# Optimization experiments

Hardware: AMD Instinct MI355X
Metric: run time of the kernel (lower is better)

## Reference

```python
import jax, jax.numpy as jnp
import numpy as np

NUM_SEQS = 16
NUM_HEADS = 32
NUM_KV_HEADS = 8
HEAD_SIZE = 128
BLOCK_SIZE = 16
X = 8  # vectorized key-cache packing factor
MAX_CTX = 4096
MAX_BLOCKS = MAX_CTX // BLOCK_SIZE
NUM_BLOCKS = NUM_SEQS * MAX_BLOCKS
SCALE = 0.08838834764831845  # 1/sqrt(128)
NEG_INF = -1e30


def setup_inputs() -> dict:
    key0 = jax.random.key(0)
    ks = jax.random.split(key0, 5)
    query = jax.random.normal(ks[0], (NUM_SEQS, 1, NUM_HEADS * HEAD_SIZE), jnp.float32)
    key = jax.random.normal(ks[1], (NUM_SEQS, 1, NUM_KV_HEADS * HEAD_SIZE), jnp.float32)
    value = jax.random.normal(ks[2], (NUM_SEQS, 1, NUM_KV_HEADS * HEAD_SIZE), jnp.float32)
    key_cache = jax.random.normal(ks[3], (NUM_BLOCKS, NUM_KV_HEADS, HEAD_SIZE // X, BLOCK_SIZE, X), jnp.float32)
    value_cache = jax.random.normal(ks[4], (NUM_BLOCKS, NUM_KV_HEADS, HEAD_SIZE, BLOCK_SIZE), jnp.float32)
    rng = np.random.default_rng(0)
    block_tables = rng.permutation(NUM_BLOCKS).reshape(NUM_SEQS, MAX_BLOCKS).astype(np.int32)
    context_lens = rng.integers(256, MAX_CTX + 1, size=(NUM_SEQS,)).astype(np.int32)
    last = context_lens - 1
    slots = block_tables[np.arange(NUM_SEQS), last // BLOCK_SIZE].astype(np.int64) * BLOCK_SIZE + (last % BLOCK_SIZE)
    slot_mapping = slots.reshape(NUM_SEQS, 1)
    return {
        'query': query, 'key': key, 'value': value,
        'key_cache': key_cache, 'value_cache': value_cache,
        'block_tables': jnp.asarray(block_tables),
        'context_lens': jnp.asarray(context_lens),
        'slot_mapping': jnp.asarray(slot_mapping),
    }


def _paged_attention_decode(query, key, value, key_cache, value_cache, block_tables, context_lens, slot_mapping):
    S, L1, hidden = query.shape  # L1 == 1 (decode)
    nb, kvH, _, bs, x = key_cache.shape
    D = value_cache.shape[2]
    H = hidden // D
    G = H // kvH  # queries per kv head
    maxB = block_tables.shape[1]

    q = query.reshape(S, H, D)
    k_new = key.reshape(S, kvH, D)
    v_new = value.reshape(S, kvH, D)

    # --- reshape_and_cache: write new K/V into paged caches ---
    sm = slot_mapping.reshape(-1)
    blk, off = sm // bs, sm % bs
    key_cache = key_cache.at[blk, :, :, off, :].set(k_new.reshape(S, kvH, D // x, x))
    value_cache = value_cache.at[blk, :, :, off].set(v_new)

    # --- gather paged KV via block tables ---
    # key_cache [nb,kvH,D/x,bs,x] -> [nb,kvH,bs,D]
    kc = key_cache.transpose(0, 1, 3, 2, 4).reshape(nb, kvH, bs, D)
    vc = value_cache.transpose(0, 1, 3, 2)  # [nb,kvH,bs,D]
    keys = kc[block_tables].transpose(0, 1, 3, 2, 4).reshape(S, maxB * bs, kvH, D)
    vals = vc[block_tables].transpose(0, 1, 3, 2, 4).reshape(S, maxB * bs, kvH, D)

    # --- GQA attention with context-length masking ---
    qg = q.reshape(S, kvH, G, D)
    scores = jnp.einsum('skgd,slkd->skgl', qg, keys) * jnp.asarray(SCALE, q.dtype)
    valid = jnp.arange(maxB * bs)[None, :] < context_lens[:, None]  # [S,L]
    scores = jnp.where(valid[:, None, None, :], scores, NEG_INF)
    probs = jax.nn.softmax(scores, axis=-1)
    out = jnp.einsum('skgl,slkd->skgd', probs, vals)
    return out.reshape(S, 1, H * D)


def reference(query, key, value, key_cache, value_cache, block_tables, context_lens, slot_mapping):
    return _paged_attention_decode(query, key, value, key_cache, value_cache,
                                   block_tables, context_lens, slot_mapping)
```

## Files before the change

kernel.cpp:

```cpp
#include <hip/hip_runtime.h>

#define NSEQ   16
#define KVH    8
#define NG     4
#define HD     128
#define BS     16
#define MAXB   256
#define PART   256
#define NPART  16
#define NITEMS (NSEQ * KVH * NPART)
#define WPT    64
#define PSTRIDE 520
#define REC_BYTES ((size_t)NITEMS * PSTRIDE * 4)
#define SCALE_F 0.08838834764831845f
#define NWORKERS 1024

__global__ __launch_bounds__(256) void pa_partial_kernel(
    const float* __restrict__ query,
    const float* __restrict__ key,
    const float* __restrict__ value,
    const float* __restrict__ key_cache,
    const float* __restrict__ value_cache,
    const int*   __restrict__ block_tables,
    const int*   __restrict__ context_lens,
    float*       __restrict__ ws,
    unsigned int* __restrict__ counter)
{
    __shared__ float p_lds[4][NG][WPT];
    __shared__ float o_lds[4][NG * HD];
    __shared__ float ml_lds[4][8];
    __shared__ int   item_s;

    const int tid  = threadIdx.x;
    const int wv   = tid >> 6;
    const int lane = tid & 63;

    for (;;) {
        if (tid == 0) item_s = (int)atomicAdd(counter, 1u);
        __syncthreads();
        const int item = item_s;
        __syncthreads();
        if (item >= NITEMS) return;

        const int p   = item & (NPART - 1);
        const int kvh = (item >> 4) & (KVH - 1);
        const int s   = item >> 7;
        const int ctx = context_lens[s];
        const int t0  = p * PART;
        if (t0 >= ctx) continue;

        const int tw0  = t0 + wv * WPT;
        const bool wact = (tw0 < ctx);

        const float* q = query + ((size_t)s * KVH + kvh) * (NG * HD);

        float m_w = -1e30f;
        float l_w[NG] = {0.f, 0.f, 0.f, 0.f};

        if (wact) {
            const int t  = tw0 + lane;
            const int bt = block_tables[s * MAXB + (t >> 4)];
            const float* kb = key_cache + (size_t)bt * (KVH * HD * BS)
                                        + (size_t)kvh * (HD * BS) + (t & 15) * 8;

            float sc[NG] = {0.f, 0.f, 0.f, 0.f};
            #pragma unroll
            for (int j = 0; j < 16; ++j) {
                const float4 ka = *(const float4*)(kb + j * 128);
                const float4 kc = *(const float4*)(kb + j * 128 + 4);
                #pragma unroll
                for (int g = 0; g < NG; ++g) {
                    sc[g] += q[g * HD + j * 8 + 0] * ka.x + q[g * HD + j * 8 + 1] * ka.y
                           + q[g * HD + j * 8 + 2] * ka.z + q[g * HD + j * 8 + 3] * ka.w
                           + q[g * HD + j * 8 + 4] * kc.x + q[g * HD + j * 8 + 5] * kc.y
                           + q[g * HD + j * 8 + 6] * kc.z + q[g * HD + j * 8 + 7] * kc.w;
                }
            }

            if (t == ctx - 1) {
                const float4* kn4 = (const float4*)(key + ((size_t)s * KVH + kvh) * HD);
                float ns[NG] = {0.f, 0.f, 0.f, 0.f};
                #pragma unroll
                for (int c = 0; c < 32; ++c) {
                    const float4 k4 = kn4[c];
                    #pragma unroll
                    for (int g = 0; g < NG; ++g) {
                        ns[g] += q[g * HD + c * 4 + 0] * k4.x + q[g * HD + c * 4 + 1] * k4.y
                               + q[g * HD + c * 4 + 2] * k4.z + q[g * HD + c * 4 + 3] * k4.w;
                    }
                }
                #pragma unroll
                for (int g = 0; g < NG; ++g) sc[g] = ns[g];
            }

            float mv;
            if (t < ctx) {
                #pragma unroll
                for (int g = 0; g < NG; ++g) sc[g] *= SCALE_F;
                mv = fmaxf(fmaxf(sc[0], sc[1]), fmaxf(sc[2], sc[3]));
            } else {
                #pragma unroll
                for (int g = 0; g < NG; ++g) sc[g] = -1e30f;
                mv = -1e30f;
            }

            #pragma unroll
            for (int o = 32; o; o >>= 1) mv = fmaxf(mv, __shfl_xor(mv, o));
            m_w = mv;

            float pr[NG];
            #pragma unroll
            for (int g = 0; g < NG; ++g) {
                pr[g] = __expf(sc[g] - m_w);
                p_lds[wv][g][lane] = pr[g];
                l_w[g] = pr[g];
            }
            #pragma unroll
            for (int o = 32; o; o >>= 1) {
                l_w[0] += __shfl_xor(l_w[0], o);
                l_w[1] += __shfl_xor(l_w[1], o);
                l_w[2] += __shfl_xor(l_w[2], o);
                l_w[3] += __shfl_xor(l_w[3], o);
            }
        }

        if (lane == 0) {
            ml_lds[wv][0] = m_w;
            #pragma unroll
            for (int g = 0; g < NG; ++g) ml_lds[wv][1 + g] = l_w[g];
        }

        if (wact) {
            int btv[4];
            #pragma unroll
            for (int b = 0; b < 4; ++b)
                btv[b] = block_tables[s * MAXB + (tw0 >> 4) + b];

            const int tl = ctx - 1 - tw0;
            const int tq = lane & 3;
            const int dl = lane >> 2;

            float acc[NG][8];
            #pragma unroll
            for (int g = 0; g < NG; ++g)
                #pragma unroll
                for (int sub = 0; sub < 8; ++sub) acc[g][sub] = 0.f;

            #pragma unroll
            for (int b = 0; b < 4; ++b) {
                if (tw0 + b * 16 < ctx) {
                    const float* vb = value_cache + (size_t)btv[b] * (KVH * HD * BS)
                                                  + (size_t)kvh * (HD * BS);
                    float4 p4[NG];
                    #pragma unroll
                    for (int g = 0; g < NG; ++g)
                        p4[g] = *(const float4*)&p_lds[wv][g][b * 16 + tq * 4];
                    #pragma unroll
                    for (int sub = 0; sub < 8; ++sub) {
                        const float4 v4 = *(const float4*)(vb + sub * 256 + lane * 4);
                        #pragma unroll
                        for (int g = 0; g < NG; ++g)
                            acc[g][sub] += p4[g].x * v4.x + p4[g].y * v4.y
                                         + p4[g].z * v4.z + p4[g].w * v4.w;
                    }
                }
            }

            #pragma unroll
            for (int g = 0; g < NG; ++g)
                #pragma unroll
                for (int sub = 0; sub < 8; ++sub) {
                    float a = acc[g][sub];
                    a += __shfl_xor(a, 1);
                    a += __shfl_xor(a, 2);
                    acc[g][sub] = a;
                }

            if (tl >= 0 && tl < WPT) {
                const int btn = block_tables[s * MAXB + ((ctx - 1) >> 4)];
                const float* vbn = value_cache + (size_t)btn * (KVH * HD * BS)
                                               + (size_t)kvh * (HD * BS) + ((ctx - 1) & 15);
                const float* vrow = value + ((size_t)s * KVH + kvh) * HD;
                #pragma unroll
                for (int sub = 0; sub < 8; ++sub) {
                    const int d = sub * 16 + dl;
                    const float dv = vrow[d] - vbn[d * BS];
                    #pragma unroll
                    for (int g = 0; g < NG; ++g)
                        acc[g][sub] += p_lds[wv][g][tl] * dv;
                }
            }

            if (tq == 0) {
                #pragma unroll
                for (int g = 0; g < NG; ++g)
                    #pragma unroll
                    for (int sub = 0; sub < 8; ++sub)
                        o_lds[wv][g * HD + sub * 16 + dl] = acc[g][sub];
            }
        } else {
            #pragma unroll
            for (int i = 0; i < 8; ++i) o_lds[wv][i * 64 + lane] = 0.f;
        }

        __syncthreads();

        const float m0 = ml_lds[0][0], m1 = ml_lds[1][0], m2 = ml_lds[2][0], m3 = ml_lds[3][0];
        const float M  = fmaxf(fmaxf(m0, m1), fmaxf(m2, m3));
        const float w0 = __expf(m0 - M), w1 = __expf(m1 - M);
        const float w2 = __expf(m2 - M), w3 = __expf(m3 - M);

        float* rec = ws + (size_t)item * PSTRIDE;
        #pragma unroll
        for (int r = 0; r < 2; ++r) {
            const int idx = tid + r * 256;
            rec[idx] = w0 * o_lds[0][idx] + w1 * o_lds[1][idx]
                     + w2 * o_lds[2][idx] + w3 * o_lds[3][idx];
        }
        if (tid < NG) {
            rec[512 + tid] = w0 * ml_lds[0][1 + tid] + w1 * ml_lds[1][1 + tid]
                           + w2 * ml_lds[2][1 + tid] + w3 * ml_lds[3][1 + tid];
        }
        if (tid == 4) rec[516] = M;
    }
}

__global__ __launch_bounds__(128) void pa_reduce_kernel(
    const float* __restrict__ ws,
    const int*   __restrict__ context_lens,
    float*       __restrict__ out)
{
    const int b    = blockIdx.x;
    const int g    = b & 3;
    const int pair = b >> 2;
    const int s    = pair >> 3;
    const int kvh  = pair & 7;
    const int ctx  = context_lens[s];
    const int np   = (ctx + PART - 1) / PART;

    const int d = threadIdx.x;
    const float* base = ws + (size_t)pair * NPART * PSTRIDE;

    float M = -1e30f;
    for (int p2 = 0; p2 < np; ++p2) M = fmaxf(M, base[p2 * PSTRIDE + 516]);

    float L = 0.f, acc = 0.f;
    for (int p2 = 0; p2 < np; ++p2) {
        const float* rec = base + p2 * PSTRIDE;
        const float w = __expf(rec[516] - M);
        L   += w * rec[512 + g];
        acc += w * rec[g * HD + d];
    }

    out[(size_t)s * (KVH * NG * HD) + (size_t)(kvh * NG + g) * HD + d] = acc / L;
}

extern "C" void kernel_launch(void* const* d_in, const int* in_sizes, int n_in,
                              void* d_out, int out_size, void* d_ws, size_t ws_size,
                              hipStream_t stream) {
    const float* query       = (const float*)d_in[0];
    const float* key         = (const float*)d_in[1];
    const float* value       = (const float*)d_in[2];
    const float* key_cache   = (const float*)d_in[3];
    const float* value_cache = (const float*)d_in[4];
    const int*   block_tables  = (const int*)d_in[5];
    const int*   context_lens  = (const int*)d_in[6];

    float* out = (float*)d_out;
    float* ws  = (float*)d_ws;
    unsigned int* counter = (unsigned int*)((char*)d_ws + REC_BYTES);

    (void)hipMemsetAsync(counter, 0, sizeof(unsigned int), stream);
    pa_partial_kernel<<<NWORKERS, 256, 0, stream>>>(
        query, key, value, key_cache, value_cache, block_tables, context_lens, ws, counter);
    pa_reduce_kernel<<<NSEQ * KVH * NG, 128, 0, stream>>>(ws, context_lens, out);
}
```

Baseline: 83.60 us.

## Fuse split-K reduction into partial kernel via per-pair completion counters

Removes the separate reduce kernel launch. Each work item bumps an atomic per-(seq,kv-head) counter, and the block that finishes the last partition merges the partial records with coherent loads and writes the output. This saves one kernel launch and its tail gap. In exchange it adds fences, atomics and an extra barrier per item, and the final merge is serialized on whichever block closes each pair.

```diff
diff --git a/kernel.cpp b/kernel.cpp
--- a/kernel.cpp
+++ b/kernel.cpp
@@ -9,13 +9,18 @@
 #define PART   256
 #define NPART  16
 #define NITEMS (NSEQ * KVH * NPART)
+#define NPAIRS (NSEQ * KVH)
 #define WPT    64
 #define PSTRIDE 520
 #define REC_BYTES ((size_t)NITEMS * PSTRIDE * 4)
 #define SCALE_F 0.08838834764831845f
 #define NWORKERS 1024
 
-__global__ __launch_bounds__(256) void pa_partial_kernel(
+__device__ __forceinline__ float cohld(const float* p) {
+    return __hip_atomic_load(p, __ATOMIC_RELAXED, __HIP_MEMORY_SCOPE_AGENT);
+}
+
+__global__ __launch_bounds__(256) void pa_fused_kernel(
     const float* __restrict__ query,
     const float* __restrict__ key,
     const float* __restrict__ value,
@@ -24,12 +29,16 @@
     const int*   __restrict__ block_tables,
     const int*   __restrict__ context_lens,
     float*       __restrict__ ws,
-    unsigned int* __restrict__ counter)
+    unsigned int* __restrict__ counter,
+    float*       __restrict__ out)
 {
     __shared__ float p_lds[4][NG][WPT];
     __shared__ float o_lds[4][NG * HD];
     __shared__ float ml_lds[4][8];
     __shared__ int   item_s;
+    __shared__ int   close_s;
+
+    unsigned int* pair_done = counter + 1;
 
     const int tid  = threadIdx.x;
     const int wv   = tid >> 6;
@@ -42,217 +51,223 @@
         __syncthreads();
         if (item >= NITEMS) return;
 
-        const int p   = item & (NPART - 1);
-        const int kvh = (item >> 4) & (KVH - 1);
-        const int s   = item >> 7;
-        const int ctx = context_lens[s];
-        const int t0  = p * PART;
-        if (t0 >= ctx) continue;
-
-        const int tw0  = t0 + wv * WPT;
-        const bool wact = (tw0 < ctx);
-
-        const float* q = query + ((size_t)s * KVH + kvh) * (NG * HD);
-
-        float m_w = -1e30f;
-        float l_w[NG] = {0.f, 0.f, 0.f, 0.f};
-
-        if (wact) {
-            const int t  = tw0 + lane;
-            const int bt = block_tables[s * MAXB + (t >> 4)];
-            const float* kb = key_cache + (size_t)bt * (KVH * HD * BS)
-                                        + (size_t)kvh * (HD * BS) + (t & 15) * 8;
-
-            float sc[NG] = {0.f, 0.f, 0.f, 0.f};
+        const int p    = item & (NPART - 1);
+        const int kvh  = (item >> 4) & (KVH - 1);
+        const int s    = item >> 7;
+        const int pair = item >> 4;
+        const int ctx  = context_lens[s];
+        const int t0   = p * PART;
+        const bool active = (t0 < ctx);
+
+        if (active) {
+            const int tw0  = t0 + wv * WPT;
+            const bool wact = (tw0 < ctx);
+
+            const float* q = query + ((size_t)s * KVH + kvh) * (NG * HD);
+
+            float m_w = -1e30f;
+            float l_w[NG] = {0.f, 0.f, 0.f, 0.f};
+
+            if (wact) {
+                const int t  = tw0 + lane;
+                const int bt = block_tables[s * MAXB + (t >> 4)];
+                const float* kb = key_cache + (size_t)bt * (KVH * HD * BS)
+                                            + (size_t)kvh * (HD * BS) + (t & 15) * 8;
+
+                float sc[NG] = {0.f, 0.f, 0.f, 0.f};
+                #pragma unroll
+                for (int j = 0; j < 16; ++j) {
+                    const float4 ka = *(const float4*)(kb + j * 128);
+                    const float4 kc = *(const float4*)(kb + j * 128 + 4);
+                    #pragma unroll
+                    for (int g = 0; g < NG; ++g) {
+                        sc[g] += q[g * HD + j * 8 + 0] * ka.x + q[g * HD + j * 8 + 1] * ka.y
+                               + q[g * HD + j * 8 + 2] * ka.z + q[g * HD + j * 8 + 3] * ka.w
+                               + q[g * HD + j * 8 + 4] * kc.x + q[g * HD + j * 8 + 5] * kc.y
+                               + q[g * HD + j * 8 + 6] * kc.z + q[g * HD + j * 8 + 7] * kc.w;
+                    }
+                }
+
+                if (t == ctx - 1) {
+                    const float4* kn4 = (const float4*)(key + ((size_t)s * KVH + kvh) * HD);
+                    float ns[NG] = {0.f, 0.f, 0.f, 0.f};
+                    #pragma unroll
+                    for (int c = 0; c < 32; ++c) {
+                        const float4 k4 = kn4[c];
+                        #pragma unroll
+                        for (int g = 0; g < NG; ++g) {
+                            ns[g] += q[g * HD + c * 4 + 0] * k4.x + q[g * HD + c * 4 + 1] * k4.y
+                                   + q[g * HD + c * 4 + 2] * k4.z + q[g * HD + c * 4 + 3] * k4.w;
+                        }
+                    }
+                    #pragma unroll
+                    for (int g = 0; g < NG; ++g) sc[g] = ns[g];
+                }
+
+                float mv;
+                if (t < ctx) {
+                    #pragma unroll
+                    for (int g = 0; g < NG; ++g) sc[g] *= SCALE_F;
+                    mv = fmaxf(fmaxf(sc[0], sc[1]), fmaxf(sc[2], sc[3]));
+                } else {
+                    #pragma unroll
+                    for (int g = 0; g < NG; ++g) sc[g] = -1e30f;
+                    mv = -1e30f;
+                }
+
+                #pragma unroll
+                for (int o = 32; o; o >>= 1) mv = fmaxf(mv, __shfl_xor(mv, o));
+                m_w = mv;
+
+                float pr[NG];
+                #pragma unroll
+                for (int g = 0; g < NG; ++g) {
+                    pr[g] = __expf(sc[g] - m_w);
+                    p_lds[wv][g][lane] = pr[g];
+                    l_w[g] = pr[g];
+                }
+                #pragma unroll
+                for (int o = 32; o; o >>= 1) {
+                    l_w[0] += __shfl_xor(l_w[0], o);
+                    l_w[1] += __shfl_xor(l_w[1], o);
+                    l_w[2] += __shfl_xor(l_w[2], o);
+                    l_w[3] += __shfl_xor(l_w[3], o);
+                }
+            }
+
+            if (lane == 0) {
+                ml_lds[wv][0] = m_w;
+                #pragma unroll
+                for (int g = 0; g < NG; ++g) ml_lds[wv][1 + g] = l_w[g];
+            }
+
+            if (wact) {
+                int btv[4];
+                #pragma unroll
+                for (int b = 0; b < 4; ++b)
+                    btv[b] = block_tables[s * MAXB + (tw0 >> 4) + b];
+
+                const int tl = ctx - 1 - tw0;
+                const int tq = lane & 3;
+                const int dl = lane >> 2;
+
+                float acc[NG][8];
+                #pragma unroll
+                for (int g = 0; g < NG; ++g)
+                    #pragma unroll
+                    for (int sub = 0; sub < 8; ++sub) acc[g][sub] = 0.f;
+
+                #pragma unroll
+                for (int b = 0; b < 4; ++b) {
+                    if (tw0 + b * 16 < ctx) {
+                        const float* vb = value_cache + (size_t)btv[b] * (KVH * HD * BS)
+                                                      + (size_t)kvh * (HD * BS);
+                        float4 p4[NG];
+                        #pragma unroll
+                        for (int g = 0; g < NG; ++g)
+                            p4[g] = *(const float4*)&p_lds[wv][g][b * 16 + tq * 4];
+                        #pragma unroll
+                        for (int sub = 0; sub < 8; ++sub) {
+                            const float4 v4 = *(const float4*)(vb + sub * 256 + lane * 4);
+                            #pragma unroll
+                            for (int g = 0; g < NG; ++g)
+                                acc[g][sub] += p4[g].x * v4.x + p4[g].y * v4.y
+                                             + p4[g].z * v4.z + p4[g].w * v4.w;
+                        }
+                    }
+                }
+
+                #pragma unroll
+                for (int g = 0; g < NG; ++g)
+                    #pragma unroll
+                    for (int sub = 0; sub < 8; ++sub) {
+                        float a = acc[g][sub];
+                        a += __shfl_xor(a, 1);
+                        a += __shfl_xor(a, 2);
+                        acc[g][sub] = a;
+                    }
+
+                if (tl >= 0 && tl < WPT) {
+                    const int btn = block_tables[s * MAXB + ((ctx - 1) >> 4)];
+                    const float* vbn = value_cache + (size_t)btn * (KVH * HD * BS)
+                                                   + (size_t)kvh * (HD * BS) + ((ctx - 1) & 15);
+                    const float* vrow = value + ((size_t)s * KVH + kvh) * HD;
+                    #pragma unroll
+                    for (int sub = 0; sub < 8; ++sub) {
+                        const int d = sub * 16 + dl;
+                        const float dv = vrow[d] - vbn[d * BS];
+                        #pragma unroll
+                        for (int g = 0; g < NG; ++g)
+                            acc[g][sub] += p_lds[wv][g][tl] * dv;
+                    }
+                }
+
+                if (tq == 0) {
+                    #pragma unroll
+                    for (int g = 0; g < NG; ++g)
+                        #pragma unroll
+                        for (int sub = 0; sub < 8; ++sub)
+                            o_lds[wv][g * HD + sub * 16 + dl] = acc[g][sub];
+                }
+            } else {
+                #pragma unroll
+                for (int i = 0; i < 8; ++i) o_lds[wv][i * 64 + lane] = 0.f;
+            }
+
+            __syncthreads();
+
+            const float m0 = ml_lds[0][0], m1 = ml_lds[1][0], m2 = ml_lds[2][0], m3 = ml_lds[3][0];
+            const float M  = fmaxf(fmaxf(m0, m1), fmaxf(m2, m3));
+            const float w0 = __expf(m0 - M), w1 = __expf(m1 - M);
+            const float w2 = __expf(m2 - M), w3 = __expf(m3 - M);
+
+            float* rec = ws + (size_t)item * PSTRIDE;
             #pragma unroll
-            for (int j = 0; j < 16; ++j) {
-                const float4 ka = *(const float4*)(kb + j * 128);
-                const float4 kc = *(const float4*)(kb + j * 128 + 4);
-                #pragma unroll
-                for (int g = 0; g < NG; ++g) {
-                    sc[g] += q[g * HD + j * 8 + 0] * ka.x + q[g * HD + j * 8 + 1] * ka.y
-                           + q[g * HD + j * 8 + 2] * ka.z + q[g * HD + j * 8 + 3] * ka.w
-                           + q[g * HD + j * 8 + 4] * kc.x + q[g * HD + j * 8 + 5] * kc.y
-                           + q[g * HD + j * 8 + 6] * kc.z + q[g * HD + j * 8 + 7] * kc.w;
-                }
-            }
-
-            if (t == ctx - 1) {
-                const float4* kn4 = (const float4*)(key + ((size_t)s * KVH + kvh) * HD);
-                float ns[NG] = {0.f, 0.f, 0.f, 0.f};
-                #pragma unroll
-                for (int c = 0; c < 32; ++c) {
-                    const float4 k4 = kn4[c];
-                    #pragma unroll
-                    for (int g = 0; g < NG; ++g) {
-                        ns[g] += q[g * HD + c * 4 + 0] * k4.x + q[g * HD + c * 4 + 1] * k4.y
-                               + q[g * HD + c * 4 + 2] * k4.z + q[g * HD + c * 4 + 3] * k4.w;
-                    }
-                }
-                #pragma unroll
-                for (int g = 0; g < NG; ++g) sc[g] = ns[g];
-            }
-
-            float mv;
-            if (t < ctx) {
-                #pragma unroll
-                for (int g = 0; g < NG; ++g) sc[g] *= SCALE_F;
-                mv = fmaxf(fmaxf(sc[0], sc[1]), fmaxf(sc[2], sc[3]));
-            } else {
-                #pragma unroll
-                for (int g = 0; g < NG; ++g) sc[g] = -1e30f;
-                mv = -1e30f;
-            }
+            for (int r = 0; r < 2; ++r) {
+                const int idx = tid + r * 256;
+                rec[idx] = w0 * o_lds[0][idx] + w1 * o_lds[1][idx]
+                         + w2 * o_lds[2][idx] + w3 * o_lds[3][idx];
+            }
+            if (tid < NG) {
+                rec[512 + tid] = w0 * ml_lds[0][1 + tid] + w1 * ml_lds[1][1 + tid]
+                               + w2 * ml_lds[2][1 + tid] + w3 * ml_lds[3][1 + tid];
+            }
+            if (tid == 4) rec[516] = M;
+
+            __syncthreads();
+        }
+
+        if (tid == 0) {
+            __threadfence();
+            const unsigned old = atomicAdd(&pair_done[pair], 1u);
+            close_s = (old == NPART - 1) ? 1 : 0;
+        }
+        __syncthreads();
+
+        if (close_s) {
+            __threadfence();
+            const int np = (ctx + PART - 1) / PART;
+            const float* base = ws + (size_t)pair * NPART * PSTRIDE;
+
+            float M = -1e30f;
+            for (int p2 = 0; p2 < np; ++p2)
+                M = fmaxf(M, cohld(base + p2 * PSTRIDE + 516));
 
             #pragma unroll
-            for (int o = 32; o; o >>= 1) mv = fmaxf(mv, __shfl_xor(mv, o));
-            m_w = mv;
-
-            float pr[NG];
-            #pragma unroll
-            for (int g = 0; g < NG; ++g) {
-                pr[g] = __expf(sc[g] - m_w);
-                p_lds[wv][g][lane] = pr[g];
-                l_w[g] = pr[g];
-            }
-            #pragma unroll
-            for (int o = 32; o; o >>= 1) {
-                l_w[0] += __shfl_xor(l_w[0], o);
-                l_w[1] += __shfl_xor(l_w[1], o);
-                l_w[2] += __shfl_xor(l_w[2], o);
-                l_w[3] += __shfl_xor(l_w[3], o);
+            for (int half = 0; half < 2; ++half) {
+                const int g = (tid >> 7) + half * 2;
+                const int d = tid & 127;
+                float L = 0.f, acc = 0.f;
+                for (int p2 = 0; p2 < np; ++p2) {
+                    const float* rec = base + p2 * PSTRIDE;
+                    const float w = __expf(cohld(rec + 516) - M);
+                    L   += w * cohld(rec + 512 + g);
+                    acc += w * cohld(rec + g * HD + d);
+                }
+                out[(size_t)s * (KVH * NG * HD) + (size_t)(kvh * NG + g) * HD + d] = acc / L;
             }
         }
-
-        if (lane == 0) {
-            ml_lds[wv][0] = m_w;
-            #pragma unroll
-            for (int g = 0; g < NG; ++g) ml_lds[wv][1 + g] = l_w[g];
-        }
-
-        if (wact) {
-            int btv[4];
-            #pragma unroll
-            for (int b = 0; b < 4; ++b)
-                btv[b] = block_tables[s * MAXB + (tw0 >> 4) + b];
-
-            const int tl = ctx - 1 - tw0;
-            const int tq = lane & 3;
-            const int dl = lane >> 2;
-
-            float acc[NG][8];
-            #pragma unroll
-            for (int g = 0; g < NG; ++g)
-                #pragma unroll
-                for (int sub = 0; sub < 8; ++sub) acc[g][sub] = 0.f;
-
-            #pragma unroll
-            for (int b = 0; b < 4; ++b) {
-                if (tw0 + b * 16 < ctx) {
-                    const float* vb = value_cache + (size_t)btv[b] * (KVH * HD * BS)
-                                                  + (size_t)kvh * (HD * BS);
-                    float4 p4[NG];
-                    #pragma unroll
-                    for (int g = 0; g < NG; ++g)
-                        p4[g] = *(const float4*)&p_lds[wv][g][b * 16 + tq * 4];
-                    #pragma unroll
-                    for (int sub = 0; sub < 8; ++sub) {
-                        const float4 v4 = *(const float4*)(vb + sub * 256 + lane * 4);
-                        #pragma unroll
-                        for (int g = 0; g < NG; ++g)
-                            acc[g][sub] += p4[g].x * v4.x + p4[g].y * v4.y
-                                         + p4[g].z * v4.z + p4[g].w * v4.w;
-                    }
-                }
-            }
-
-            #pragma unroll
-            for (int g = 0; g < NG; ++g)
-                #pragma unroll
-                for (int sub = 0; sub < 8; ++sub) {
-                    float a = acc[g][sub];
-                    a += __shfl_xor(a, 1);
-                    a += __shfl_xor(a, 2);
-                    acc[g][sub] = a;
-                }
-
-            if (tl >= 0 && tl < WPT) {
-                const int btn = block_tables[s * MAXB + ((ctx - 1) >> 4)];
-                const float* vbn = value_cache + (size_t)btn * (KVH * HD * BS)
-                                               + (size_t)kvh * (HD * BS) + ((ctx - 1) & 15);
-                const float* vrow = value + ((size_t)s * KVH + kvh) * HD;
-                #pragma unroll
-                for (int sub = 0; sub < 8; ++sub) {
-                    const int d = sub * 16 + dl;
-                    const float dv = vrow[d] - vbn[d * BS];
-                    #pragma unroll
-                    for (int g = 0; g < NG; ++g)
-                        acc[g][sub] += p_lds[wv][g][tl] * dv;
-                }
-            }
-
-            if (tq == 0) {
-                #pragma unroll
-                for (int g = 0; g < NG; ++g)
-                    #pragma unroll
-                    for (int sub = 0; sub < 8; ++sub)
-                        o_lds[wv][g * HD + sub * 16 + dl] = acc[g][sub];
-            }
-        } else {
-            #pragma unroll
-            for (int i = 0; i < 8; ++i) o_lds[wv][i * 64 + lane] = 0.f;
-        }
-
-        __syncthreads();
-
-        const float m0 = ml_lds[0][0], m1 = ml_lds[1][0], m2 = ml_lds[2][0], m3 = ml_lds[3][0];
-        const float M  = fmaxf(fmaxf(m0, m1), fmaxf(m2, m3));
-        const float w0 = __expf(m0 - M), w1 = __expf(m1 - M);
-        const float w2 = __expf(m2 - M), w3 = __expf(m3 - M);
-
-        float* rec = ws + (size_t)item * PSTRIDE;
-        #pragma unroll
-        for (int r = 0; r < 2; ++r) {
-            const int idx = tid + r * 256;
-            rec[idx] = w0 * o_lds[0][idx] + w1 * o_lds[1][idx]
-                     + w2 * o_lds[2][idx] + w3 * o_lds[3][idx];
-        }
-        if (tid < NG) {
-            rec[512 + tid] = w0 * ml_lds[0][1 + tid] + w1 * ml_lds[1][1 + tid]
-                           + w2 * ml_lds[2][1 + tid] + w3 * ml_lds[3][1 + tid];
-        }
-        if (tid == 4) rec[516] = M;
     }
-}
-
-__global__ __launch_bounds__(128) void pa_reduce_kernel(
-    const float* __restrict__ ws,
-    const int*   __restrict__ context_lens,
-    float*       __restrict__ out)
-{
-    const int b    = blockIdx.x;
-    const int g    = b & 3;
-    const int pair = b >> 2;
-    const int s    = pair >> 3;
-    const int kvh  = pair & 7;
-    const int ctx  = context_lens[s];
-    const int np   = (ctx + PART - 1) / PART;
-
-    const int d = threadIdx.x;
-    const float* base = ws + (size_t)pair * NPART * PSTRIDE;
-
-    float M = -1e30f;
-    for (int p2 = 0; p2 < np; ++p2) M = fmaxf(M, base[p2 * PSTRIDE + 516]);
-
-    float L = 0.f, acc = 0.f;
-    for (int p2 = 0; p2 < np; ++p2) {
-        const float* rec = base + p2 * PSTRIDE;
-        const float w = __expf(rec[516] - M);
-        L   += w * rec[512 + g];
-        acc += w * rec[g * HD + d];
-    }
-
-    out[(size_t)s * (KVH * NG * HD) + (size_t)(kvh * NG + g) * HD + d] = acc / L;
 }
 
 extern "C" void kernel_launch(void* const* d_in, const int* in_sizes, int n_in,
@@ -270,8 +285,8 @@
     float* ws  = (float*)d_ws;
     unsigned int* counter = (unsigned int*)((char*)d_ws + REC_BYTES);
 
-    (void)hipMemsetAsync(counter, 0, sizeof(unsigned int), stream);
-    pa_partial_kernel<<<NWORKERS, 256, 0, stream>>>(
-        query, key, value, key_cache, value_cache, block_tables, context_lens, ws, counter);
-    pa_reduce_kernel<<<NSEQ * KVH * NG, 128, 0, stream>>>(ws, context_lens, out);
+    (void)hipMemsetAsync(counter, 0, (1 + NPAIRS) * sizeof(unsigned int), stream);
+    pa_fused_kernel<<<NWORKERS, 256, 0, stream>>>(
+        query, key, value, key_cache, value_cache, block_tables, context_lens,
+        ws, counter, out);
 }
```

Result: slower. 212.8 us (+154.6%).
